# Kernel tuning notes

Measured on AMD Instinct MI355X. Metric: run time of the kernel, lower is better.

The kernel has to match this reference:

```python
import jax, jax.numpy as jnp
import numpy as np

NP_, NC_, F_, H_ = 50000, 10000, 128, 256
E_ANN, E_LINK, E_PPI, NPAIR = 400000, 160000, 800000, 200000


def _edges(key, E, n_src, n_dst):
    # random edges with src != dst (PyG GATConv removes then re-adds self loops;
    # generating none keeps the edge set fixed under that transform)
    k1, k2 = jax.random.split(key)
    src = jax.random.randint(k1, (E,), 0, n_src)
    dst = (src + 1 + jax.random.randint(k2, (E,), 0, n_dst - 1)) % n_dst
    return jnp.stack([src, dst]).astype(jnp.int32)


def setup_inputs() -> dict:
    key = jax.random.key(0)
    ks = jax.random.split(key, 20)
    g = lambda k, shape, s: jax.random.normal(k, shape, dtype=jnp.float32) * s
    sF, sH = 1.0 / np.sqrt(F_), 1.0 / np.sqrt(H_)
    inp = {}
    inp['xp'] = g(ks[0], (NP_, F_), 1.0)
    inp['xc'] = g(ks[1], (NC_, F_), 1.0)
    inp['ei_pann'] = _edges(ks[2], E_ANN, NP_, NC_)
    inp['ei_nann'] = _edges(ks[3], E_ANN, NP_, NC_)
    inp['ei_link'] = _edges(ks[4], E_LINK, NC_, NC_)
    inp['ei_ppi'] = _edges(ks[5], E_PPI, NP_, NP_)
    inp['mask'] = jax.random.randint(ks[6], (NPAIR, 2), 0, NP_).astype(jnp.int32)
    # GAT params, stacked over edge types [0]=+annotation, [1]=-annotation, [2]=ppi
    inp['Wa'] = g(ks[7], (3, F_, H_), sF)
    inp['att_src_a'] = g(ks[8], (3, H_), sH)
    inp['att_dst_a'] = g(ks[9], (3, H_), sH)
    inp['bias_a'] = jnp.zeros((3, H_), jnp.float32)
    inp['Wb'] = g(ks[10], (3, H_, F_), sH)
    inp['att_src_b'] = g(ks[11], (3, F_), sF)
    inp['att_dst_b'] = g(ks[12], (3, F_), sF)
    inp['bias_b'] = jnp.zeros((3, F_), jnp.float32)
    # GraphConv (class->class) params
    inp['Wrel_a'] = g(ks[13], (F_, H_), sF)
    inp['Wroot_a'] = g(ks[14], (F_, H_), sF)
    inp['brel_a'] = jnp.zeros((H_,), jnp.float32)
    inp['Wrel_b'] = g(ks[15], (H_, F_), sH)
    inp['Wroot_b'] = g(ks[16], (H_, F_), sH)
    inp['brel_b'] = jnp.zeros((F_,), jnp.float32)
    inp['W_out'] = g(ks[17], (2 * F_, 1), 1.0 / np.sqrt(2 * F_))
    inp['b_out'] = jnp.zeros((1,), jnp.float32)
    return inp


def _gat(x_src, x_dst, ei, W, a_s, a_d, b):
    # PyG GATConv, heads=1, negative_slope=0.2, add_self_loops=True (num_nodes=min)
    n_src, n_dst = x_src.shape[0], x_dst.shape[0]
    loops = jnp.arange(min(n_src, n_dst), dtype=ei.dtype)
    src = jnp.concatenate([ei[0], loops])
    dst = jnp.concatenate([ei[1], loops])
    hs = x_src @ W                                     # [N_src, out]
    hd = x_dst @ W                                     # [N_dst, out]
    e = jax.nn.leaky_relu((hs @ a_s)[src] + (hd @ a_d)[dst], 0.2)  # [E]
    m = jax.ops.segment_max(e, dst, num_segments=n_dst)
    ex = jnp.exp(e - m[dst])
    denom = jax.ops.segment_sum(ex, dst, num_segments=n_dst)
    alpha = ex / denom[dst]                            # segment softmax over dst
    out = jax.ops.segment_sum(alpha[:, None] * hs[src], dst, num_segments=n_dst)
    return out + b


def _graph_conv(x, ei, W_rel, W_root, b_rel):
    # PyG GraphConv, aggr='add': lin_rel(sum_j x_j) + lin_root(x_i)
    agg = jax.ops.segment_sum(x[ei[0]], ei[1], num_segments=x.shape[0])
    return agg @ W_rel + b_rel + x @ W_root


def reference(xp, xc, ei_pann, ei_nann, ei_link, ei_ppi, mask,
              Wa, att_src_a, att_dst_a, bias_a,
              Wb, att_src_b, att_dst_b, bias_b,
              Wrel_a, Wroot_a, brel_a, Wrel_b, Wroot_b, brel_b,
              W_out, b_out):
    # ---- HeteroConv layer a (sum-aggregate over edge types per dst type) ----
    hc = (_gat(xp, xc, ei_pann, Wa[0], att_src_a[0], att_dst_a[0], bias_a[0])
          + _gat(xp, xc, ei_nann, Wa[1], att_src_a[1], att_dst_a[1], bias_a[1])
          + _graph_conv(xc, ei_link, Wrel_a, Wroot_a, brel_a))
    hp = _gat(xp, xp, ei_ppi, Wa[2], att_src_a[2], att_dst_a[2], bias_a[2])
    hc = jax.nn.relu(hc)  # dropout p=0.0 -> identity
    hp = jax.nn.relu(hp)
    # ---- HeteroConv layer b ----
    hc2 = (_gat(hp, hc, ei_pann, Wb[0], att_src_b[0], att_dst_b[0], bias_b[0])
           + _gat(hp, hc, ei_nann, Wb[1], att_src_b[1], att_dst_b[1], bias_b[1])
           + _graph_conv(hc, ei_link, Wrel_b, Wroot_b, brel_b))
    del hc2  # class embeddings are computed but unused by the original forward
    hp2 = _gat(hp, hp, ei_ppi, Wb[2], att_src_b[2], att_dst_b[2], bias_b[2])
    # ---- link prediction head ----
    mT = mask.T
    p1 = jax.lax.stop_gradient(hp2[mT[0]])  # .detach() in the original
    p2 = jax.lax.stop_gradient(hp2[mT[1]])
    h = jnp.concatenate([p1, p2], axis=1)   # [n_pairs, 2*F]
    return jax.nn.sigmoid(h @ W_out + b_out)
```

## Files before the change

kernel.cpp:

```cpp
#include <hip/hip_runtime.h>
#include <hip/hip_bf16.h>
#include <math.h>

#define NP 50000
#define F 128
#define H 256
#define E_PPI 800000
#define ET (E_PPI + NP)
#define NPAIR 200000
#define CAP 96
#define FILL_BLOCKS ((ET + 255) / 256)

typedef __attribute__((ext_vector_type(8))) short short8v;
typedef __attribute__((ext_vector_type(4))) float float4v;
typedef __attribute__((ext_vector_type(2))) float float2v;
typedef __attribute__((ext_vector_type(4))) unsigned int uint4v;

__device__ __forceinline__ short f2bs(float f) {
  unsigned u = __builtin_bit_cast(unsigned, f);
  unsigned r = (u + 0x7FFFu + ((u >> 16) & 1u)) >> 16;
  return (short)r;
}
__device__ __forceinline__ float bs2f(short s) {
  unsigned u = ((unsigned)(unsigned short)s) << 16;
  return __builtin_bit_cast(float, u);
}
__device__ __forceinline__ float lrelu(float t) { return (t > 0.f) ? t : 0.2f * t; }

__device__ __forceinline__ float2v bf2x2(unsigned d) {
  float2v f;
  f.x = __builtin_bit_cast(float, d << 16);
  f.y = __builtin_bit_cast(float, d & 0xFFFF0000u);
  return f;
}
__device__ __forceinline__ float2v pkfma(float2v a, float2v b, float2v c) {
#if __has_builtin(__builtin_elementwise_fma)
  return __builtin_elementwise_fma(a, b, c);
#else
  float2v r; r.x = fmaf(a.x, b.x, c.x); r.y = fmaf(a.y, b.y, c.y); return r;
#endif
}


template<int K, int N>
__device__ __forceinline__ void pack_one(const float* __restrict__ B, short* __restrict__ Bp,
                                         int idx) {
  constexpr int KB = K / 32;
  int lane = idx & 63;
  int rest = idx >> 6;
  int kb = rest % KB;
  int tile = rest / KB;
  int n = tile * 16 + (lane & 15);
  int k0 = kb * 32 + (lane >> 4) * 8;
  size_t base = (size_t)idx * 8;
#pragma unroll
  for (int j = 0; j < 8; ++j) Bp[base + j] = f2bs(B[(size_t)(k0 + j) * N + n]);
}

__global__ void fill_pack(const int* __restrict__ src_idx, const int* __restrict__ dst_idx,
                          int* __restrict__ deg, int* __restrict__ bucket,
                          const float* __restrict__ Wa, short* __restrict__ BaP,
                          const float* __restrict__ Wb, const float* __restrict__ asb,
                          const float* __restrict__ adb, const float* __restrict__ Wout,
                          float* __restrict__ wvec,
                          const float* __restrict__ bb, float* __restrict__ consts) {
  int b = blockIdx.x;
  if (b < FILL_BLOCKS) {
    int k = b * 256 + threadIdx.x;
    if (k >= ET) return;
    int s, d;
    if (k < E_PPI) { s = src_idx[k]; d = dst_idx[k]; }
    else           { s = d = k - E_PPI; }
    int pos = atomicAdd(&deg[d], 1);
    if (pos < CAP) bucket[(size_t)d * CAP + pos] = s;
  } else if (b < FILL_BLOCKS + 16) {
    int idx = (b - FILL_BLOCKS) * 256 + threadIdx.x;
    pack_one<F, H>(Wa, BaP, idx);
  } else if (b < FILL_BLOCKS + 20) {
    int t = (b - FILL_BLOCKS - 16) * 256 + threadIdx.x;
    int vec = t >> 8, k = t & 255;
    const float* srcv = (vec == 0) ? asb : (vec == 1) ? adb
                      : (vec == 2) ? Wout : (Wout + F);
    const float* wrow = Wb + (size_t)k * F;
    float acc = 0.f;
#pragma unroll 4
    for (int j = 0; j < F; ++j) acc = fmaf(wrow[j], srcv[j], acc);
    wvec[vec * 256 + k] = acc;
  } else {
    int lane = threadIdx.x;
    if (lane >= 64) return;
    float b0 = bb[lane], b1 = bb[lane + 64];
    float c1 = fmaf(b0, Wout[lane], b1 * Wout[lane + 64]);
    float c2 = fmaf(b0, Wout[128 + lane], b1 * Wout[192 + lane]);
#pragma unroll
    for (int o = 32; o; o >>= 1) {
      c1 += __shfl_xor(c1, o);
      c2 += __shfl_xor(c2, o);
    }
    if (lane == 0) { consts[0] = c1; consts[1] = c2; }
  }
}


__launch_bounds__(256)
__global__ void gemm_a(const float* __restrict__ A, const short* __restrict__ Bp,
                       short* __restrict__ Cb, const float* __restrict__ a_s,
                       const float* __restrict__ a_d, float* __restrict__ sb,
                       float* __restrict__ db) {
  constexpr int K = F, N = H;
  constexpr int KB = K / 32;
  constexpr int TPW = N / 64;
  __shared__ float sred[4][16];
  __shared__ float dred[4][16];
  int lane = threadIdx.x & 63, wave = threadIdx.x >> 6;
  int ln16 = lane & 15, quad = lane >> 4;
  int m0 = blockIdx.x * 16;
  float4v acc[TPW];
#pragma unroll
  for (int t = 0; t < TPW; ++t) acc[t] = (float4v)0.f;
#pragma unroll
  for (int kb = 0; kb < KB; ++kb) {
    int ka = kb * 32 + quad * 8;
    const float* ap = A + (size_t)(m0 + ln16) * K + ka;
    float4v a0 = *(const float4v*)ap;
    float4v a1 = *(const float4v*)(ap + 4);
    short8v ah;
#pragma unroll
    for (int j = 0; j < 4; ++j) { ah[j] = f2bs(a0[j]); ah[4 + j] = f2bs(a1[j]); }
#pragma unroll
    for (int t = 0; t < TPW; ++t) {
      int tile = wave * TPW + t;
      short8v bh = *(const short8v*)(Bp + ((size_t)(tile * KB + kb) * 64 + lane) * 8);
      acc[t] = __builtin_amdgcn_mfma_f32_16x16x32_bf16(ah, bh, acc[t], 0, 0, 0);
    }
  }
#pragma unroll
  for (int t = 0; t < TPW; ++t) {
    int cc = (wave * TPW + t) * 16 + ln16;
#pragma unroll
    for (int r = 0; r < 4; ++r) {
      int rr = m0 + quad * 4 + r;
      Cb[(size_t)rr * N + cc] = f2bs(acc[t][r]);
    }
  }
  float su[4] = {0.f, 0.f, 0.f, 0.f}, dv[4] = {0.f, 0.f, 0.f, 0.f};
#pragma unroll
  for (int t = 0; t < TPW; ++t) {
    int cc = (wave * TPW + t) * 16 + ln16;
    float as = a_s[cc], ad = a_d[cc];
#pragma unroll
    for (int r = 0; r < 4; ++r) {
      su[r] = fmaf(acc[t][r], as, su[r]);
      dv[r] = fmaf(acc[t][r], ad, dv[r]);
    }
  }
#pragma unroll
  for (int r = 0; r < 4; ++r) {
    for (int off = 1; off < 16; off <<= 1) {
      su[r] += __shfl_xor(su[r], off);
      dv[r] += __shfl_xor(dv[r], off);
    }
  }
  if (ln16 == 0) {
#pragma unroll
    for (int r = 0; r < 4; ++r) {
      sred[wave][quad * 4 + r] = su[r];
      dred[wave][quad * 4 + r] = dv[r];
    }
  }
  __syncthreads();
  if (threadIdx.x < 16) {
    int row = threadIdx.x;
    sb[m0 + row] = sred[0][row] + sred[1][row] + sred[2][row] + sred[3][row];
    db[m0 + row] = dred[0][row] + dred[1][row] + dred[2][row] + dred[3][row];
  }
}


__launch_bounds__(256)
__global__ void agg_a(const short* __restrict__ h, const int* __restrict__ bucket,
                      const int* __restrict__ degv, const float* __restrict__ sb,
                      const float* __restrict__ db, const float* __restrict__ bias,
                      const float* __restrict__ wvec,
                      float* __restrict__ sb2, float* __restrict__ db2,
                      float2v* __restrict__ pq) {
  int gid = blockIdx.x * blockDim.x + threadIdx.x;
  int dst = gid >> 6, lane = gid & 63;
  if (dst >= NP) return;
  int half = lane >> 5, l32 = lane & 31;
  const int* row = bucket + (size_t)dst * CAP;
  int deg = degv[dst];
  float di = db[dst];
  float m = -1e30f, ssum = 0.f, x0 = -1e30f;
  for (int c0 = 0; c0 < deg; c0 += 64) {
    int idx = c0 + lane;
    float x = -1e30f;
    if (idx < deg) x = lrelu(sb[row[idx]] + di);
    if (c0 == 0) x0 = x;
    float cm = x;
#pragma unroll
    for (int o = 32; o; o >>= 1) cm = fmaxf(cm, __shfl_xor(cm, o));
    float nm = fmaxf(m, cm);
    float ex = (idx < deg) ? __expf(x - nm) : 0.f;
#pragma unroll
    for (int o = 32; o; o >>= 1) ex += __shfl_xor(ex, o);
    ssum = ssum * __expf(m - nm) + ex;
    m = nm;
  }
  float inv = 1.0f / ssum;
  float w0 = __expf(x0 - m);
  float2v acc2[4];
#pragma unroll
  for (int k = 0; k < 4; ++k) acc2[k] = (float2v)0.f;
  for (int it0 = 0; it0 < deg; it0 += 4) {
    int e1 = it0 + half, e2 = it0 + 2 + half;
    bool v1 = (e1 < deg), v2 = (e2 < deg);
    int s1 = v1 ? row[e1] : row[0];
    int s2 = v2 ? row[e2] : row[0];
    short8v xa = *(const short8v*)(h + (size_t)s1 * 256 + l32 * 8);
    short8v xb = *(const short8v*)(h + (size_t)s2 * 256 + l32 * 8);
    float w1 = __shfl(w0, e1 & 63);
    float w2 = __shfl(w0, e2 & 63);
    if (deg > 64) {
      if (e1 >= 64 && v1) w1 = __expf(lrelu(sb[s1] + di) - m);
      if (e2 >= 64 && v2) w2 = __expf(lrelu(sb[s2] + di) - m);
    }
    w1 = v1 ? w1 : 0.f;
    w2 = v2 ? w2 : 0.f;
    uint4v da = __builtin_bit_cast(uint4v, xa);
    uint4v dbv = __builtin_bit_cast(uint4v, xb);
    float2v W1 = {w1, w1}, W2 = {w2, w2};
#pragma unroll
    for (int k = 0; k < 4; ++k) {
      acc2[k] = pkfma(bf2x2(da[k]), W1, acc2[k]);
      acc2[k] = pkfma(bf2x2(dbv[k]), W2, acc2[k]);
    }
  }
#pragma unroll
  for (int k = 0; k < 4; ++k) {
    acc2[k].x += __shfl_xor(acc2[k].x, 32);
    acc2[k].y += __shfl_xor(acc2[k].y, 32);
  }
  float ts = 0.f, td = 0.f, tp = 0.f, tq = 0.f;
#pragma unroll
  for (int k = 0; k < 4; ++k) {
#pragma unroll
    for (int half_c = 0; half_c < 2; ++half_c) {
      int c = l32 * 8 + 2 * k + half_c;
      float a = half_c ? acc2[k].y : acc2[k].x;
      float o = fmaxf(fmaf(a, inv, bias[c]), 0.f);
      ts = fmaf(o, wvec[c], ts);
      td = fmaf(o, wvec[256 + c], td);
      tp = fmaf(o, wvec[512 + c], tp);
      tq = fmaf(o, wvec[768 + c], tq);
    }
  }
#pragma unroll
  for (int o = 1; o < 32; o <<= 1) {
    ts += __shfl_xor(ts, o);
    td += __shfl_xor(td, o);
    tp += __shfl_xor(tp, o);
    tq += __shfl_xor(tq, o);
  }
  if (lane == 0) {
    sb2[dst] = ts;
    db2[dst] = td;
    float2v t; t.x = tp; t.y = tq;
    pq[dst] = t;
  }
}


__launch_bounds__(256)
__global__ void agg_uv(const int* __restrict__ bucket, const int* __restrict__ degv,
                       const float* __restrict__ sb, const float* __restrict__ db,
                       const float2v* __restrict__ pq, float* __restrict__ u,
                       float* __restrict__ v_out) {
  int gid = blockIdx.x * blockDim.x + threadIdx.x;
  int dst = gid >> 6, lane = gid & 63;
  if (dst >= NP) return;
  const int* row = bucket + (size_t)dst * CAP;
  int deg = degv[dst];
  float di = db[dst];
  float m = -1e30f, ssum = 0.f, uacc = 0.f, vacc = 0.f;
  for (int c0 = 0; c0 < deg; c0 += 64) {
    int idx = c0 + lane;
    bool val = idx < deg;
    int src = val ? row[idx] : row[0];
    float x = val ? lrelu(sb[src] + di) : -1e30f;
    float2v pqv = pq[src];
    float cm = x;
#pragma unroll
    for (int o = 32; o; o >>= 1) cm = fmaxf(cm, __shfl_xor(cm, o));
    float nm = fmaxf(m, cm);
    float scale = __expf(m - nm);
    float ex = val ? __expf(x - nm) : 0.f;
    float eu = ex * pqv.x, ev = ex * pqv.y;
#pragma unroll
    for (int o = 32; o; o >>= 1) {
      ex += __shfl_xor(ex, o);
      eu += __shfl_xor(eu, o);
      ev += __shfl_xor(ev, o);
    }
    ssum = ssum * scale + ex;
    uacc = uacc * scale + eu;
    vacc = vacc * scale + ev;
    m = nm;
  }
  if (lane == 0) {
    float inv = 1.0f / ssum;
    u[dst] = uacc * inv;
    v_out[dst] = vacc * inv;
  }
}


__global__ void out_kernel(const int* __restrict__ mask, const float* __restrict__ u,
                           const float* __restrict__ v, const float* __restrict__ bout,
                           const float* __restrict__ consts, float* __restrict__ out) {
  int p = blockIdx.x * blockDim.x + threadIdx.x;
  if (p >= NPAIR) return;
  int a = mask[2 * p], b = mask[2 * p + 1];
  float logit = u[a] + v[b] + bout[0] + consts[0] + consts[1];
  out[p] = 1.0f / (1.0f + __expf(-logit));
}


extern "C" void kernel_launch(void* const* d_in, const int* in_sizes, int n_in,
                              void* d_out, int out_size, void* d_ws, size_t ws_size,
                              hipStream_t stream) {
  const float* xp   = (const float*)d_in[0];
  const int*   ei   = (const int*)d_in[5];
  const int*   mask = (const int*)d_in[6];
  const float* Wa2  = (const float*)d_in[7]  + 2 * F * H;
  const float* asa  = (const float*)d_in[8]  + 2 * H;
  const float* ada  = (const float*)d_in[9]  + 2 * H;
  const float* ba   = (const float*)d_in[10] + 2 * H;
  const float* Wb2  = (const float*)d_in[11] + 2 * H * F;
  const float* asb  = (const float*)d_in[12] + 2 * F;
  const float* adb  = (const float*)d_in[13] + 2 * F;
  const float* bb   = (const float*)d_in[14] + 2 * F;
  const float* Wout = (const float*)d_in[21];
  const float* bout = (const float*)d_in[22];
  float* out = (float*)d_out;

  char* ws = (char*)d_ws;
  size_t off = 0;
  auto alloc = [&](size_t bytes) {
    void* p = ws + off;
    off = (off + bytes + 255) & ~(size_t)255;
    return p;
  };
  short* h1b     = (short*)alloc((size_t)NP * H * 2);
  int*   bucket  = (int*)alloc((size_t)NP * CAP * 4);
  int*   deg     = (int*)alloc((size_t)NP * 4);
  float* sb      = (float*)alloc((size_t)NP * 4);
  float* db      = (float*)alloc((size_t)NP * 4);
  float* sb2     = (float*)alloc((size_t)NP * 4);
  float* db2     = (float*)alloc((size_t)NP * 4);
  float2v* pq    = (float2v*)alloc((size_t)NP * 8);
  float* u       = (float*)alloc((size_t)NP * 4);
  float* v       = (float*)alloc((size_t)NP * 4);
  short* BaP     = (short*)alloc((size_t)F * H * 2);
  float* wvec    = (float*)alloc(4 * 256 * 4);
  float* consts  = (float*)alloc(2 * 4);

  const int* src_idx = ei;
  const int* dst_idx = ei + E_PPI;

  hipMemsetAsync(deg, 0, (size_t)NP * 4, stream);
  fill_pack<<<FILL_BLOCKS + 21, 256, 0, stream>>>(src_idx, dst_idx, deg, bucket,
                                                  Wa2, BaP, Wb2, asb, adb, Wout,
                                                  wvec, bb, consts);

  int node_wave_blocks = NP / 4;

  gemm_a<<<NP / 16, 256, 0, stream>>>(xp, BaP, h1b, asa, ada, sb, db);
  agg_a<<<node_wave_blocks, 256, 0, stream>>>(h1b, bucket, deg, sb, db, ba,
                                              wvec, sb2, db2, pq);
  agg_uv<<<node_wave_blocks, 256, 0, stream>>>(bucket, deg, sb2, db2, pq, u, v);
  out_kernel<<<(NPAIR + 255) / 256, 256, 0, stream>>>(mask, u, v, bout, consts, out);
}
```

Baseline: 284.6 us.

## Fuse projection GEMM into edge-bucketing prep kernel, drop weight pack pass

Merges the layer-a projection GEMM (with its attention score reductions) into the same launch as the edge bucketing and constant-vector setup, so one kernel launch and the pack-then-GEMM dependency go away. Each GEMM block now converts the Wa weights to bf16 fragments in registers straight from fp32 and reuses them across 5 row tiles of 16 rows, instead of reading a pre-packed buffer. agg_a also stages wvec in shared memory. The risks are heavy register pressure from holding 16 B fragments, strided uncoalesced weight reads repeated in every GEMM block, and mixing atomic fill blocks with MFMA blocks in a single grid.

```diff
diff --git a/kernel.cpp b/kernel.cpp
--- a/kernel.cpp
+++ b/kernel.cpp
@@ -10,6 +10,8 @@
 #define NPAIR 200000
 #define CAP 96
 #define FILL_BLOCKS ((ET + 255) / 256)
+#define GROWS 80
+#define GB (NP / GROWS)
 
 typedef __attribute__((ext_vector_type(8))) short short8v;
 typedef __attribute__((ext_vector_type(4))) float float4v;
@@ -42,28 +44,18 @@
 }
 
 
-template<int K, int N>
-__device__ __forceinline__ void pack_one(const float* __restrict__ B, short* __restrict__ Bp,
-                                         int idx) {
-  constexpr int KB = K / 32;
-  int lane = idx & 63;
-  int rest = idx >> 6;
-  int kb = rest % KB;
-  int tile = rest / KB;
-  int n = tile * 16 + (lane & 15);
-  int k0 = kb * 32 + (lane >> 4) * 8;
-  size_t base = (size_t)idx * 8;
-#pragma unroll
-  for (int j = 0; j < 8; ++j) Bp[base + j] = f2bs(B[(size_t)(k0 + j) * N + n]);
-}
-
-__global__ void fill_pack(const int* __restrict__ src_idx, const int* __restrict__ dst_idx,
-                          int* __restrict__ deg, int* __restrict__ bucket,
-                          const float* __restrict__ Wa, short* __restrict__ BaP,
-                          const float* __restrict__ Wb, const float* __restrict__ asb,
-                          const float* __restrict__ adb, const float* __restrict__ Wout,
-                          float* __restrict__ wvec,
-                          const float* __restrict__ bb, float* __restrict__ consts) {
+__global__ __launch_bounds__(256)
+void prep(const int* __restrict__ src_idx, const int* __restrict__ dst_idx,
+          int* __restrict__ deg, int* __restrict__ bucket,
+          const float* __restrict__ xp, const float* __restrict__ Wa,
+          short* __restrict__ h1b, const float* __restrict__ a_s,
+          const float* __restrict__ a_d, float* __restrict__ sb,
+          float* __restrict__ db, const float* __restrict__ Wb,
+          const float* __restrict__ asb, const float* __restrict__ adb,
+          const float* __restrict__ Wout, float* __restrict__ wvec,
+          const float* __restrict__ bb, float* __restrict__ consts) {
+  __shared__ float sred[4][16];
+  __shared__ float dred[4][16];
   int b = blockIdx.x;
   if (b < FILL_BLOCKS) {
     int k = b * 256 + threadIdx.x;
@@ -73,11 +65,85 @@
     else           { s = d = k - E_PPI; }
     int pos = atomicAdd(&deg[d], 1);
     if (pos < CAP) bucket[(size_t)d * CAP + pos] = s;
-  } else if (b < FILL_BLOCKS + 16) {
-    int idx = (b - FILL_BLOCKS) * 256 + threadIdx.x;
-    pack_one<F, H>(Wa, BaP, idx);
-  } else if (b < FILL_BLOCKS + 20) {
-    int t = (b - FILL_BLOCKS - 16) * 256 + threadIdx.x;
+  } else if (b < FILL_BLOCKS + GB) {
+    int gb = b - FILL_BLOCKS;
+    int lane = threadIdx.x & 63, wave = threadIdx.x >> 6;
+    int ln16 = lane & 15, quad = lane >> 4;
+    short8v bf[16];
+#pragma unroll
+    for (int kb = 0; kb < 4; ++kb) {
+      int k0 = kb * 32 + quad * 8;
+#pragma unroll
+      for (int t = 0; t < 4; ++t) {
+        int n = (wave * 4 + t) * 16 + ln16;
+        const float* wp_ = Wa + (size_t)k0 * H + n;
+        short8v vf;
+#pragma unroll
+        for (int j = 0; j < 8; ++j) vf[j] = f2bs(wp_[(size_t)j * H]);
+        bf[kb * 4 + t] = vf;
+      }
+    }
+    for (int rt = 0; rt < 5; ++rt) {
+      int m0 = gb * GROWS + rt * 16;
+      float4v acc[4];
+#pragma unroll
+      for (int t = 0; t < 4; ++t) acc[t] = (float4v)0.f;
+#pragma unroll
+      for (int kb = 0; kb < 4; ++kb) {
+        const float* ap = xp + (size_t)(m0 + ln16) * F + kb * 32 + quad * 8;
+        float4v a0 = *(const float4v*)ap;
+        float4v a1 = *(const float4v*)(ap + 4);
+        short8v ah;
+#pragma unroll
+        for (int j = 0; j < 4; ++j) { ah[j] = f2bs(a0[j]); ah[4 + j] = f2bs(a1[j]); }
+#pragma unroll
+        for (int t = 0; t < 4; ++t)
+          acc[t] = __builtin_amdgcn_mfma_f32_16x16x32_bf16(ah, bf[kb * 4 + t], acc[t], 0, 0, 0);
+      }
+#pragma unroll
+      for (int t = 0; t < 4; ++t) {
+        int cc = (wave * 4 + t) * 16 + ln16;
+#pragma unroll
+        for (int r = 0; r < 4; ++r) {
+          int rr = m0 + quad * 4 + r;
+          h1b[(size_t)rr * H + cc] = f2bs(acc[t][r]);
+        }
+      }
+      float su[4] = {0.f, 0.f, 0.f, 0.f}, dv[4] = {0.f, 0.f, 0.f, 0.f};
+#pragma unroll
+      for (int t = 0; t < 4; ++t) {
+        int cc = (wave * 4 + t) * 16 + ln16;
+        float as = a_s[cc], ad = a_d[cc];
+#pragma unroll
+        for (int r = 0; r < 4; ++r) {
+          su[r] = fmaf(acc[t][r], as, su[r]);
+          dv[r] = fmaf(acc[t][r], ad, dv[r]);
+        }
+      }
+#pragma unroll
+      for (int r = 0; r < 4; ++r) {
+        for (int off = 1; off < 16; off <<= 1) {
+          su[r] += __shfl_xor(su[r], off);
+          dv[r] += __shfl_xor(dv[r], off);
+        }
+      }
+      if (ln16 == 0) {
+#pragma unroll
+        for (int r = 0; r < 4; ++r) {
+          sred[wave][quad * 4 + r] = su[r];
+          dred[wave][quad * 4 + r] = dv[r];
+        }
+      }
+      __syncthreads();
+      if (threadIdx.x < 16) {
+        int row = threadIdx.x;
+        sb[m0 + row] = sred[0][row] + sred[1][row] + sred[2][row] + sred[3][row];
+        db[m0 + row] = dred[0][row] + dred[1][row] + dred[2][row] + dred[3][row];
+      }
+      __syncthreads();
+    }
+  } else if (b < FILL_BLOCKS + GB + 4) {
+    int t = (b - FILL_BLOCKS - GB) * 256 + threadIdx.x;
     int vec = t >> 8, k = t & 255;
     const float* srcv = (vec == 0) ? asb : (vec == 1) ? adb
                       : (vec == 2) ? Wout : (Wout + F);
@@ -103,90 +169,17 @@
 
 
 __launch_bounds__(256)
-__global__ void gemm_a(const float* __restrict__ A, const short* __restrict__ Bp,
-                       short* __restrict__ Cb, const float* __restrict__ a_s,
-                       const float* __restrict__ a_d, float* __restrict__ sb,
-                       float* __restrict__ db) {
-  constexpr int K = F, N = H;
-  constexpr int KB = K / 32;
-  constexpr int TPW = N / 64;
-  __shared__ float sred[4][16];
-  __shared__ float dred[4][16];
-  int lane = threadIdx.x & 63, wave = threadIdx.x >> 6;
-  int ln16 = lane & 15, quad = lane >> 4;
-  int m0 = blockIdx.x * 16;
-  float4v acc[TPW];
-#pragma unroll
-  for (int t = 0; t < TPW; ++t) acc[t] = (float4v)0.f;
-#pragma unroll
-  for (int kb = 0; kb < KB; ++kb) {
-    int ka = kb * 32 + quad * 8;
-    const float* ap = A + (size_t)(m0 + ln16) * K + ka;
-    float4v a0 = *(const float4v*)ap;
-    float4v a1 = *(const float4v*)(ap + 4);
-    short8v ah;
-#pragma unroll
-    for (int j = 0; j < 4; ++j) { ah[j] = f2bs(a0[j]); ah[4 + j] = f2bs(a1[j]); }
-#pragma unroll
-    for (int t = 0; t < TPW; ++t) {
-      int tile = wave * TPW + t;
-      short8v bh = *(const short8v*)(Bp + ((size_t)(tile * KB + kb) * 64 + lane) * 8);
-      acc[t] = __builtin_amdgcn_mfma_f32_16x16x32_bf16(ah, bh, acc[t], 0, 0, 0);
-    }
-  }
-#pragma unroll
-  for (int t = 0; t < TPW; ++t) {
-    int cc = (wave * TPW + t) * 16 + ln16;
-#pragma unroll
-    for (int r = 0; r < 4; ++r) {
-      int rr = m0 + quad * 4 + r;
-      Cb[(size_t)rr * N + cc] = f2bs(acc[t][r]);
-    }
-  }
-  float su[4] = {0.f, 0.f, 0.f, 0.f}, dv[4] = {0.f, 0.f, 0.f, 0.f};
-#pragma unroll
-  for (int t = 0; t < TPW; ++t) {
-    int cc = (wave * TPW + t) * 16 + ln16;
-    float as = a_s[cc], ad = a_d[cc];
-#pragma unroll
-    for (int r = 0; r < 4; ++r) {
-      su[r] = fmaf(acc[t][r], as, su[r]);
-      dv[r] = fmaf(acc[t][r], ad, dv[r]);
-    }
-  }
-#pragma unroll
-  for (int r = 0; r < 4; ++r) {
-    for (int off = 1; off < 16; off <<= 1) {
-      su[r] += __shfl_xor(su[r], off);
-      dv[r] += __shfl_xor(dv[r], off);
-    }
-  }
-  if (ln16 == 0) {
-#pragma unroll
-    for (int r = 0; r < 4; ++r) {
-      sred[wave][quad * 4 + r] = su[r];
-      dred[wave][quad * 4 + r] = dv[r];
-    }
-  }
-  __syncthreads();
-  if (threadIdx.x < 16) {
-    int row = threadIdx.x;
-    sb[m0 + row] = sred[0][row] + sred[1][row] + sred[2][row] + sred[3][row];
-    db[m0 + row] = dred[0][row] + dred[1][row] + dred[2][row] + dred[3][row];
-  }
-}
-
-
-__launch_bounds__(256)
 __global__ void agg_a(const short* __restrict__ h, const int* __restrict__ bucket,
                       const int* __restrict__ degv, const float* __restrict__ sb,
                       const float* __restrict__ db, const float* __restrict__ bias,
                       const float* __restrict__ wvec,
                       float* __restrict__ sb2, float* __restrict__ db2,
                       float2v* __restrict__ pq) {
+  __shared__ float wv[1024];
+  for (int i = threadIdx.x; i < 1024; i += 256) wv[i] = wvec[i];
+  __syncthreads();
   int gid = blockIdx.x * blockDim.x + threadIdx.x;
   int dst = gid >> 6, lane = gid & 63;
-  if (dst >= NP) return;
   int half = lane >> 5, l32 = lane & 31;
   const int* row = bucket + (size_t)dst * CAP;
   int deg = degv[dst];
@@ -245,14 +238,14 @@
 #pragma unroll
   for (int k = 0; k < 4; ++k) {
 #pragma unroll
-    for (int half_c = 0; half_c < 2; ++half_c) {
-      int c = l32 * 8 + 2 * k + half_c;
-      float a = half_c ? acc2[k].y : acc2[k].x;
+    for (int hc = 0; hc < 2; ++hc) {
+      int c = l32 * 8 + 2 * k + hc;
+      float a = hc ? acc2[k].y : acc2[k].x;
       float o = fmaxf(fmaf(a, inv, bias[c]), 0.f);
-      ts = fmaf(o, wvec[c], ts);
-      td = fmaf(o, wvec[256 + c], td);
-      tp = fmaf(o, wvec[512 + c], tp);
-      tq = fmaf(o, wvec[768 + c], tq);
+      ts = fmaf(o, wv[c], ts);
+      td = fmaf(o, wv[256 + c], td);
+      tp = fmaf(o, wv[512 + c], tp);
+      tq = fmaf(o, wv[768 + c], tq);
     }
   }
 #pragma unroll
@@ -361,7 +354,6 @@
   float2v* pq    = (float2v*)alloc((size_t)NP * 8);
   float* u       = (float*)alloc((size_t)NP * 4);
   float* v       = (float*)alloc((size_t)NP * 4);
-  short* BaP     = (short*)alloc((size_t)F * H * 2);
   float* wvec    = (float*)alloc(4 * 256 * 4);
   float* consts  = (float*)alloc(2 * 4);
 
@@ -369,15 +361,11 @@
   const int* dst_idx = ei + E_PPI;
 
   hipMemsetAsync(deg, 0, (size_t)NP * 4, stream);
-  fill_pack<<<FILL_BLOCKS + 21, 256, 0, stream>>>(src_idx, dst_idx, deg, bucket,
-                                                  Wa2, BaP, Wb2, asb, adb, Wout,
-                                                  wvec, bb, consts);
-
-  int node_wave_blocks = NP / 4;
-
-  gemm_a<<<NP / 16, 256, 0, stream>>>(xp, BaP, h1b, asa, ada, sb, db);
-  agg_a<<<node_wave_blocks, 256, 0, stream>>>(h1b, bucket, deg, sb, db, ba,
-                                              wvec, sb2, db2, pq);
-  agg_uv<<<node_wave_blocks, 256, 0, stream>>>(bucket, deg, sb2, db2, pq, u, v);
+  prep<<<FILL_BLOCKS + GB + 5, 256, 0, stream>>>(
+      src_idx, dst_idx, deg, bucket, xp, Wa2, h1b, asa, ada, sb, db,
+      Wb2, asb, adb, Wout, wvec, bb, consts);
+  agg_a<<<NP / 4, 256, 0, stream>>>(h1b, bucket, deg, sb, db, ba,
+                                    wvec, sb2, db2, pq);
+  agg_uv<<<NP / 4, 256, 0, stream>>>(bucket, deg, sb2, db2, pq, u, v);
   out_kernel<<<(NPAIR + 255) / 256, 256, 0, stream>>>(mask, u, v, bout, consts, out);
 }
```

Result: slower. 293.3 us (+3.1%).
